# Performance work log

Hardware: AMD Instinct MI355X
Metric: run time of the kernel (lower is better)

Reference implementation:

```python
import jax, jax.numpy as jnp
import numpy as np

N_HF = 128
N_RBF = 50
CUTOFF = 5.0
L = 3          # n_interactions
MAX_Z = 100
N_NODES = 30   # atoms per molecule
B = 1024       # molecules
N = B * N_NODES          # 30720 atoms
E = B * N_NODES * (N_NODES - 1)  # 890880 edges
N_REACT = 256
LOG2 = float(np.log(2.0))


def ssp(x):  # shifted softplus
    return jax.nn.softplus(x) - LOG2


def setup_inputs() -> dict:
    key = jax.random.key(0)
    ks = jax.random.split(key, 24)
    s = 0.02
    z = jax.random.randint(ks[0], (N,), 0, MAX_Z)
    coord = jax.random.normal(ks[1], (N, 3), jnp.float32) * 3.0
    # fully-connected edges within each molecule
    base = np.arange(N_NODES)
    row_l, col_l = np.meshgrid(base, base, indexing='ij')
    mask = row_l != col_l
    row_l, col_l = row_l[mask], col_l[mask]  # [n_nodes*(n_nodes-1)]
    offs = (np.arange(B) * N_NODES)[:, None]
    row = (offs + row_l[None, :]).reshape(-1)
    col = (offs + col_l[None, :]).reshape(-1)
    edge_index = jnp.asarray(np.stack([row, col]), jnp.int32)  # [2,E]
    atom_mask = jnp.ones((N, 1), jnp.float32)
    edge_mask = jnp.ones((E, 1), jnp.float32)
    reaction_indexes = jax.random.randint(ks[2], (B,), 0, N_REACT)
    reaction_indexes_signs = jnp.ones((B,), jnp.float32)
    # parameters
    emb = (jax.random.normal(ks[3], (MAX_Z, N_HF), jnp.float32)).at[0].set(0.0)  # padding_idx=0
    p = lambda k, shp: jax.random.normal(k, shp, jnp.float32) * s
    params = dict(
        in2f_W=p(ks[4], (L, N_HF, N_HF)),
        f_W1=p(ks[5], (L, N_RBF, N_HF)), f_b1=jnp.zeros((L, N_HF), jnp.float32),
        f_W2=p(ks[6], (L, N_HF, N_HF)), f_b2=jnp.zeros((L, N_HF), jnp.float32),
        o_W1=p(ks[7], (L, N_HF, N_HF)), o_b1=jnp.zeros((L, N_HF), jnp.float32),
        o_W2=p(ks[8], (L, N_HF, N_HF)), o_b2=jnp.zeros((L, N_HF), jnp.float32),
        dec_W1=p(ks[9], (N_HF, N_HF // 2)), dec_b1=jnp.zeros((N_HF // 2,), jnp.float32),
        dec_W2=p(ks[10], (N_HF // 2, 1)), dec_b2=jnp.zeros((1,), jnp.float32),
    )
    return dict(z=z, coord=coord, edge_index=edge_index, atom_mask=atom_mask,
                edge_mask=edge_mask, reaction_indexes=reaction_indexes,
                reaction_indexes_signs=reaction_indexes_signs, emb=emb,
                n_nodes=N_NODES, n_reactions=N_REACT, **params)


def reference(z, coord, edge_index, atom_mask, edge_mask, reaction_indexes,
              reaction_indexes_signs, emb, in2f_W, f_W1, f_b1, f_W2, f_b2,
              o_W1, o_b1, o_W2, o_b2, dec_W1, dec_b1, dec_W2, dec_b2,
              n_nodes, n_reactions):
    row, col = edge_index[0], edge_index[1]
    radial = jnp.linalg.norm(coord[row] - coord[col], axis=1)  # [E]
    h = emb[z]  # [N, n_hf]
    # GaussianRBF expansion
    offsets = jnp.linspace(0.0, CUTOFF, N_RBF)
    coeff = -0.5 / (offsets[1] - offsets[0]) ** 2
    rbf = jnp.exp(coeff * (radial[:, None] - offsets[None, :]) ** 2)  # [E, n_rbf]
    rbf = rbf * edge_mask
    # Cosine cutoff
    dc = 0.5 * (jnp.cos(radial * jnp.pi / CUTOFF) + 1.0) * (radial < CUTOFF)
    dist_cut = dc[:, None] * edge_mask  # [E,1]
    n_atoms = h.shape[0]
    for l in range(L):
        xf = h @ in2f_W[l]                                      # in2f (no bias)
        Wij = ssp(rbf @ f_W1[l] + f_b1[l]) @ f_W2[l] + f_b2[l]  # filter network
        Wij = Wij * dist_cut
        x_ij = xf[col] * Wij                                    # gather + multiply
        m = jax.ops.segment_sum(x_ij, row, num_segments=n_atoms)  # scatter-add
        m = ssp(m @ o_W1[l] + o_b1[l]) @ o_W2[l] + o_b2[l]      # f2out
        h = h + m
    h = h * atom_mask
    h = h.reshape(-1, n_nodes, N_HF).sum(axis=1)                # [B, n_hf]
    temp = ssp(h @ dec_W1 + dec_b1) @ dec_W2 + dec_b2           # [B, 1]
    pred = jnp.zeros((n_reactions,), jnp.float32).at[reaction_indexes].add(
        temp[:, 0] * reaction_indexes_signs)
    return pred
```

## Files before the change

kernel.cpp:

```cpp
#include <hip/hip_runtime.h>
#include <math.h>

#define NHF 128
#define NRBF 50
#define LAYERS 3
#define CUTOFF_F 5.0f
#define STEP_F (CUTOFF_F/49.0f)
#define LOG2_F 0.6931471805599453f
#define PI_F 3.14159265358979323846f
#define TBL 4096
#define TROWS (TBL+1)
#define TINV ((float)TBL / CUTOFF_F)

typedef __attribute__((ext_vector_type(8))) _Float16 fp16x8;
typedef __attribute__((ext_vector_type(4))) float f32x4;
typedef _Float16 f16x2 __attribute__((ext_vector_type(2)));

static __device__ __forceinline__ unsigned short f2h(float f){
    return __builtin_bit_cast(unsigned short, (_Float16)f);
}
static __device__ __forceinline__ unsigned packh(float lo, float hi){
    return (unsigned)f2h(lo) | ((unsigned)f2h(hi) << 16);
}
static __device__ __forceinline__ float sspf(float x){
    float t = exp2f(-fabsf(x) * 1.44269504f);
    return fmaxf(x, 0.0f) + 0.69314718f * (log2f(1.0f + t) - 1.0f);
}
static __device__ __forceinline__ float4 ld4(const float* p){ return *reinterpret_cast<const float4*>(p); }

__global__ __launch_bounds__(256) void k_pack(const float* __restrict__ in2f_W, const float* __restrict__ o_W1,
                                              const float* __restrict__ o_W2, uint4* __restrict__ Wp){
    int tid = blockIdx.x * 256 + threadIdx.x;
    if (tid >= 9 * 2048) return;
    int g = tid >> 11;
    int rem = tid & 2047;
    int s = rem >> 9;
    int f = (rem >> 6) & 7;
    int l = rem & 63;
    int layer = g / 3, type = g % 3;
    const float* src = (type == 0 ? in2f_W : (type == 1 ? o_W1 : o_W2)) + (size_t)layer * NHF * NHF;
    int row0 = s * 32 + ((l >> 4) << 3);
    int col  = (f << 4) + (l & 15);
    unsigned p0, p1, p2, p3;
    p0 = (unsigned)f2h(src[(row0+0)*NHF + col]) | ((unsigned)f2h(src[(row0+1)*NHF + col]) << 16);
    p1 = (unsigned)f2h(src[(row0+2)*NHF + col]) | ((unsigned)f2h(src[(row0+3)*NHF + col]) << 16);
    p2 = (unsigned)f2h(src[(row0+4)*NHF + col]) | ((unsigned)f2h(src[(row0+5)*NHF + col]) << 16);
    p3 = (unsigned)f2h(src[(row0+6)*NHF + col]) | ((unsigned)f2h(src[(row0+7)*NHF + col]) << 16);
    Wp[tid] = make_uint4(p0, p1, p2, p3);
}

__global__ __launch_bounds__(256) void k_table(const float* __restrict__ W1, const float* __restrict__ b1,
                                               const float* __restrict__ W2, const float* __restrict__ b2,
                                               unsigned short* __restrict__ Th){
    __shared__ float rbfL[2][4][52];
    __shared__ float hidL[2][4][128];
    int l = blockIdx.y;
    int tid = threadIdx.x;
    int g = tid >> 7, c = tid & 127;
    const float* W1l = W1 + (size_t)l * NRBF * NHF;
    const float* W2l = W2 + (size_t)l * NHF * NHF;
    int t0 = blockIdx.x * 8 + g * 4;
    const float coeff = -0.5f / (STEP_F * STEP_F) * 1.44269504f;
    const float dr = CUTOFF_F / (float)TBL;
    if (c < NRBF){
        float off = c * STEP_F;
        #pragma unroll
        for (int i = 0; i < 4; i++){
            int t = t0 + i; if (t > TBL) t = TBL;
            float d = t * dr - off;
            rbfL[g][i][c] = exp2f(coeff * d * d);
        }
    }
    __syncthreads();
    float acc[4];
    float bc = b1[l * NHF + c];
    #pragma unroll
    for (int i = 0; i < 4; i++) acc[i] = bc;
    #pragma unroll 5
    for (int j = 0; j < NRBF; j++){
        float wv = W1l[j * NHF + c];
        #pragma unroll
        for (int i = 0; i < 4; i++) acc[i] = fmaf(rbfL[g][i][j], wv, acc[i]);
    }
    #pragma unroll
    for (int i = 0; i < 4; i++) hidL[g][i][c] = sspf(acc[i]);
    __syncthreads();
    float b2c = b2[l * NHF + c];
    #pragma unroll
    for (int i = 0; i < 4; i++) acc[i] = b2c;
    #pragma unroll 4
    for (int j = 0; j < NHF; j++){
        float wv = W2l[j * NHF + c];
        #pragma unroll
        for (int i = 0; i < 4; i++) acc[i] = fmaf(hidL[g][i][j], wv, acc[i]);
    }
    #pragma unroll
    for (int i = 0; i < 4; i++){
        int t = t0 + i; if (t > TBL) t = TBL;
        float r = t * dr;
        float dc = (t >= TBL) ? 0.0f : 0.5f * (cosf(r * (PI_F / CUTOFF_F)) + 1.0f);
        float v = acc[i] * dc;
        Th[((size_t)l * TROWS + t) * NHF + c] = f2h(v);
    }
}

static __device__ __forceinline__ fp16x8 ldX(const unsigned* A_u, int rfbase, int ks, int l){
    int row = rfbase + (l & 15);
    int wc = ks * 16 + ((l >> 4) << 2);
    uint4 v = *reinterpret_cast<const uint4*>(&A_u[row * 64 + (wc ^ ((row & 7) << 2))]);
    return __builtin_bit_cast(fp16x8, v);
}
static __device__ __forceinline__ fp16x8 ldW(const uint4* __restrict__ Wp, int g, int ks, int cfg, int l){
    uint4 v = Wp[(((g << 2) + ks) * 8 + cfg) * 64 + l];
    return __builtin_bit_cast(fp16x8, v);
}

template<int EPI>
static __device__ __forceinline__ void gemm_phase(const uint4* __restrict__ Wp, int g,
                                                  const unsigned* A_u, uint2* D2,
                                                  float hreg[2][2][4], const float* __restrict__ bias,
                                                  int w, int l){
    f32x4 acc00 = {0,0,0,0}, acc01 = {0,0,0,0}, acc10 = {0,0,0,0}, acc11 = {0,0,0,0};
    #pragma unroll
    for (int ks = 0; ks < 4; ks++){
        fp16x8 wa0 = ldW(Wp, g, ks, w * 2 + 0, l);
        fp16x8 wa1 = ldW(Wp, g, ks, w * 2 + 1, l);
        fp16x8 xb0 = ldX(A_u, 0, ks, l);
        fp16x8 xb1 = ldX(A_u, 16, ks, l);
        acc00 = __builtin_amdgcn_mfma_f32_16x16x32_f16(wa0, xb0, acc00, 0, 0, 0);
        acc01 = __builtin_amdgcn_mfma_f32_16x16x32_f16(wa0, xb1, acc01, 0, 0, 0);
        acc10 = __builtin_amdgcn_mfma_f32_16x16x32_f16(wa1, xb0, acc10, 0, 0, 0);
        acc11 = __builtin_amdgcn_mfma_f32_16x16x32_f16(wa1, xb1, acc11, 0, 0, 0);
    }
    #pragma unroll
    for (int chf = 0; chf < 2; chf++){
        int ch0 = (w * 2 + chf) * 16 + ((l >> 4) << 2);
        float4 bv = {0,0,0,0};
        if (EPI >= 1) bv = ld4(bias + ch0);
        #pragma unroll
        for (int af = 0; af < 2; af++){
            f32x4 a = (chf == 0) ? (af == 0 ? acc00 : acc01) : (af == 0 ? acc10 : acc11);
            int atom = af * 16 + (l & 15);
            float v0 = a[0] + bv.x, v1 = a[1] + bv.y, v2 = a[2] + bv.z, v3 = a[3] + bv.w;
            if (EPI == 1){ v0 = sspf(v0); v1 = sspf(v1); v2 = sspf(v2); v3 = sspf(v3); }
            if (EPI == 2){
                v0 += hreg[chf][af][0]; hreg[chf][af][0] = v0;
                v1 += hreg[chf][af][1]; hreg[chf][af][1] = v1;
                v2 += hreg[chf][af][2]; hreg[chf][af][2] = v2;
                v3 += hreg[chf][af][3]; hreg[chf][af][3] = v3;
            }
            D2[(atom << 5) + (((ch0 >> 2) ^ ((atom & 7) << 1)))] = make_uint2(packh(v0, v1), packh(v2, v3));
        }
    }
}

__global__ __launch_bounds__(256, 4) void k_mega(const int* __restrict__ z, const float* __restrict__ coord,
                                                 const float* __restrict__ emask, const float* __restrict__ amask,
                                                 const float* __restrict__ emb,
                                                 const uint4* __restrict__ Wp,
                                                 const float* __restrict__ o_b1, const float* __restrict__ o_b2,
                                                 const unsigned* __restrict__ Tb,
                                                 const float* __restrict__ dW1, const float* __restrict__ db1,
                                                 const float* __restrict__ dW2, const float* __restrict__ db2,
                                                 float* __restrict__ tempv, int nn){
    __shared__ __align__(16) unsigned hbf[32 * 64];
    __shared__ __align__(16) unsigned xfb[32 * 64];
    __shared__ __align__(16) unsigned mbu[32 * 64];
    __shared__ __align__(16) int pkE[32 * 32];
    __shared__ int      cntL[32];
    __shared__ int      cntQ[8];
    __shared__ int      zL[32];
    __shared__ unsigned maskL[32];
    __shared__ float    cxyz[96];
    __shared__ float    amL[32];
    __shared__ float    hsb[NHF];

    int mol = blockIdx.x;
    int tid = threadIdx.x;
    int w = tid >> 6, l = tid & 63;
    int molA = mol * nn;
    int km = nn - 1;
    int ne = nn * km;

    uint2* hbf2 = reinterpret_cast<uint2*>(hbf);
    uint2* xfb2 = reinterpret_cast<uint2*>(xfb);

    if (tid < 32){ maskL[tid] = 0u; cntL[tid] = 0; }
    if (tid < 3 * nn) cxyz[tid] = coord[(size_t)molA * 3 + tid];
    if (tid < 32)     amL[tid] = (tid < nn) ? amask[molA + tid] : 0.0f;
    if (tid < 32)     zL[tid]  = (tid < nn) ? z[molA + tid] : 0;
    __syncthreads();
    for (int e = tid; e < ne; e += 256){
        if (emask[(size_t)molA * km + e] != 0.0f){
            int a = e / km, k = e - a * km;
            atomicOr(&maskL[a], 1u << k);
        }
    }

    float hreg[2][2][4];
    #pragma unroll
    for (int chf = 0; chf < 2; chf++){
        int ch0 = (w * 2 + chf) * 16 + ((l >> 4) << 2);
        #pragma unroll
        for (int af = 0; af < 2; af++){
            int atom = af * 16 + (l & 15);
            float4 v = {0,0,0,0};
            if (atom < nn) v = ld4(emb + (size_t)zL[atom] * NHF + ch0);
            hreg[chf][af][0] = v.x; hreg[chf][af][1] = v.y;
            hreg[chf][af][2] = v.z; hreg[chf][af][3] = v.w;
            hbf2[(atom << 5) + (((ch0 >> 2) ^ ((atom & 7) << 1)))] = make_uint2(packh(v.x, v.y), packh(v.z, v.w));
        }
    }
    __syncthreads();

    if (tid < nn){
        int ai = tid;
        unsigned msk = maskL[ai];
        float ax = cxyz[ai*3], ay = cxyz[ai*3+1], az = cxyz[ai*3+2];
        int cnt = 0;
        for (int k = 0; k < km; k++){
            int nb = k + (k >= ai ? 1 : 0);
            float dx = ax - cxyz[nb*3], dy = ay - cxyz[nb*3+1], dz = az - cxyz[nb*3+2];
            float r = sqrtf(dx*dx + dy*dy + dz*dz);
            int t = (int)(r * TINV + 0.5f);
            if (((msk >> k) & 1u) && t < TBL){
                pkE[ai * 32 + cnt] = nb | (t << 8);
                cnt++;
            }
        }
        cntL[ai] = cnt;
    }
    __syncthreads();
    if (tid < 32){
        int b4 = tid & ~3;
        int m0 = cntL[b4], m1 = cntL[b4+1], m2 = cntL[b4+2], m3 = cntL[b4+3];
        int mx = max(max(m0, m1), max(m2, m3));
        mx = (mx + 3) & ~3;
        for (int k = cntL[tid]; k < mx; k++) pkE[tid * 32 + k] = (TBL << 8);
        if (!(tid & 3)) cntQ[tid >> 2] = mx;
    }
    __syncthreads();

    int j16 = l & 15, g16 = l >> 4;
    for (int L = 0; L < LAYERS; L++){
        gemm_phase<0>(Wp, L * 3 + 0, hbf, xfb2, hreg, o_b1, w, l);
        __syncthreads();
        const char* Tlj = (const char*)(Tb + (size_t)L * TROWS * 64) + (j16 << 4);
        for (int q = w; q < 8; q += 4){
            int a = (q << 2) + g16;
            int n4 = cntQ[q] >> 2;
            const int4* pe4 = reinterpret_cast<const int4*>(&pkE[a * 32]);
            float accf[8] = {0,0,0,0,0,0,0,0};
            for (int k4 = 0; k4 < n4; k4++){
                int4 pv = pe4[k4];
                #pragma unroll
                for (int jj = 0; jj < 4; jj++){
                    int p = (jj == 0) ? pv.x : (jj == 1) ? pv.y : (jj == 2) ? pv.z : pv.w;
                    uint4 tw = *reinterpret_cast<const uint4*>(Tlj + (p & ~0xFF));
                    int ca = p & 31;
                    uint4 xw = *reinterpret_cast<const uint4*>(&xfb[(ca << 6) + ((j16 ^ (ca & 7)) << 2)]);
                    f16x2 t0 = __builtin_bit_cast(f16x2, tw.x), t1 = __builtin_bit_cast(f16x2, tw.y);
                    f16x2 t2 = __builtin_bit_cast(f16x2, tw.z), t3 = __builtin_bit_cast(f16x2, tw.w);
                    f16x2 x0 = __builtin_bit_cast(f16x2, xw.x), x1 = __builtin_bit_cast(f16x2, xw.y);
                    f16x2 x2 = __builtin_bit_cast(f16x2, xw.z), x3 = __builtin_bit_cast(f16x2, xw.w);
                    accf[0] += (float)t0[0] * (float)x0[0];
                    accf[1] += (float)t0[1] * (float)x0[1];
                    accf[2] += (float)t1[0] * (float)x1[0];
                    accf[3] += (float)t1[1] * (float)x1[1];
                    accf[4] += (float)t2[0] * (float)x2[0];
                    accf[5] += (float)t2[1] * (float)x2[1];
                    accf[6] += (float)t3[0] * (float)x3[0];
                    accf[7] += (float)t3[1] * (float)x3[1];
                }
            }
            *reinterpret_cast<uint4*>(&mbu[(a << 6) + ((j16 ^ (a & 7)) << 2)]) =
                make_uint4(packh(accf[0], accf[1]), packh(accf[2], accf[3]),
                           packh(accf[4], accf[5]), packh(accf[6], accf[7]));
        }
        __syncthreads();
        gemm_phase<1>(Wp, L * 3 + 1, mbu, xfb2, hreg, o_b1 + L * NHF, w, l);
        __syncthreads();
        gemm_phase<2>(Wp, L * 3 + 2, xfb, hbf2, hreg, o_b2 + L * NHF, w, l);
        __syncthreads();
    }

    {
        float s[2][4];
        #pragma unroll
        for (int chf = 0; chf < 2; chf++)
            #pragma unroll
            for (int r = 0; r < 4; r++)
                s[chf][r] = hreg[chf][0][r] * amL[l & 15] + hreg[chf][1][r] * amL[16 + (l & 15)];
        #pragma unroll
        for (int o = 1; o < 16; o <<= 1){
            #pragma unroll
            for (int chf = 0; chf < 2; chf++)
                #pragma unroll
                for (int r = 0; r < 4; r++)
                    s[chf][r] += __shfl_xor(s[chf][r], o);
        }
        if (!(l & 15)){
            #pragma unroll
            for (int chf = 0; chf < 2; chf++)
                #pragma unroll
                for (int r = 0; r < 4; r++)
                    hsb[(w * 2 + chf) * 16 + ((l >> 4) << 2) + r] = s[chf][r];
        }
    }
    __syncthreads();
    {
        float* red = (float*)pkE;
        int o = tid & 63, part = tid >> 6;
        float u = 0.0f;
        #pragma unroll 8
        for (int c = part * 32; c < part * 32 + 32; c++)
            u = fmaf(hsb[c], dW1[c * 64 + o], u);
        red[part * 64 + o] = u;
    }
    __syncthreads();
    if (tid < 64){
        float u = ((float*)pkE)[tid] + ((float*)pkE)[64 + tid] + ((float*)pkE)[128 + tid]
                + ((float*)pkE)[192 + tid] + db1[tid];
        float p = sspf(u) * dW2[tid];
        #pragma unroll
        for (int o = 32; o > 0; o >>= 1) p += __shfl_down(p, o);
        if (tid == 0) tempv[mol] = p + db2[0];
    }
}

__global__ __launch_bounds__(256) void k_pred(const float* __restrict__ tempv, const int* __restrict__ ridx,
                                              const float* __restrict__ rsign, float* __restrict__ pred,
                                              int nmol, int nreact){
    extern __shared__ float sh[];
    float* tv = sh;
    int*   ri = (int*)(sh + nmol);
    int tid = threadIdx.x;
    for (int i = tid; i < nmol; i += 256){
        tv[i] = tempv[i] * rsign[i];
        ri[i] = ridx[i];
    }
    __syncthreads();
    int r = blockIdx.x * 256 + tid;
    if (r >= nreact) return;
    float s = 0.0f;
    int i = 0;
    for (; i + 8 <= nmol; i += 8){
        #pragma unroll
        for (int j = 0; j < 8; j++){
            float v = tv[i + j];
            s += (ri[i + j] == r) ? v : 0.0f;
        }
    }
    for (; i < nmol; i++)
        s += (ri[i] == r) ? tv[i] : 0.0f;
    pred[r] = s;
}

extern "C" void kernel_launch(void* const* d_in, const int* in_sizes, int n_in,
                              void* d_out, int out_size, void* d_ws, size_t ws_size,
                              hipStream_t stream){
    const int*   z      = (const int*)  d_in[0];
    const float* coord  = (const float*)d_in[1];
    const float* amask  = (const float*)d_in[3];
    const float* emask  = (const float*)d_in[4];
    const int*   ridx   = (const int*)  d_in[5];
    const float* rsign  = (const float*)d_in[6];
    const float* emb    = (const float*)d_in[7];
    const float* in2f_W = (const float*)d_in[10];
    const float* f_W1   = (const float*)d_in[11];
    const float* f_b1   = (const float*)d_in[12];
    const float* f_W2   = (const float*)d_in[13];
    const float* f_b2   = (const float*)d_in[14];
    const float* o_W1   = (const float*)d_in[15];
    const float* o_b1   = (const float*)d_in[16];
    const float* o_W2   = (const float*)d_in[17];
    const float* o_b2   = (const float*)d_in[18];
    const float* dW1    = (const float*)d_in[19];
    const float* db1    = (const float*)d_in[20];
    const float* dW2    = (const float*)d_in[21];
    const float* db2    = (const float*)d_in[22];

    const int N  = in_sizes[0];
    const int B  = in_sizes[5];
    const int nn = N / B;
    (void)n_in; (void)ws_size;

    uint4*    Wp    = (uint4*)d_ws;
    unsigned* Tb    = (unsigned*)((char*)d_ws + 9 * 2048 * 16);
    float*    tempv = (float*)((char*)Tb + (size_t)LAYERS * TROWS * 256);

    k_pack <<<72, 256, 0, stream>>>(in2f_W, o_W1, o_W2, Wp);
    k_table<<<dim3((TROWS + 7) / 8, LAYERS), 256, 0, stream>>>(f_W1, f_b1, f_W2, f_b2,
                                                               (unsigned short*)Tb);
    k_mega <<<B, 256, 0, stream>>>(z, coord, emask, amask, emb, Wp, o_b1, o_b2, Tb,
                                   dW1, db1, dW2, db2, tempv, nn);
    k_pred <<<(out_size + 255) / 256, 256, B * 8, stream>>>(tempv, ridx, rsign,
                                                            (float*)d_out, B, out_size);
}
```

Measured before the change: 102.2 us.

## Fuse weight-pack into table kernel and interleave two atom streams per wave

The weight-packing kernel is folded into the filter-table kernel as an extra grid row, which removes one kernel launch. In the message-passing loop, each wave now handles two atoms (a and a+16) at once with independent accumulators. Previously it looped over two quads one after the other. This exposes more independent table and LDS loads for latency hiding. Padding counts are now taken as the max over 8 atoms instead of 4, so there can be more wasted padded iterations. There is also more register pressure.

```diff
diff --git a/kernel.cpp b/kernel.cpp
--- a/kernel.cpp
+++ b/kernel.cpp
@@ -28,32 +28,48 @@
 }
 static __device__ __forceinline__ float4 ld4(const float* p){ return *reinterpret_cast<const float4*>(p); }
 
-__global__ __launch_bounds__(256) void k_pack(const float* __restrict__ in2f_W, const float* __restrict__ o_W1,
-                                              const float* __restrict__ o_W2, uint4* __restrict__ Wp){
-    int tid = blockIdx.x * 256 + threadIdx.x;
-    if (tid >= 9 * 2048) return;
-    int g = tid >> 11;
-    int rem = tid & 2047;
-    int s = rem >> 9;
-    int f = (rem >> 6) & 7;
-    int l = rem & 63;
-    int layer = g / 3, type = g % 3;
-    const float* src = (type == 0 ? in2f_W : (type == 1 ? o_W1 : o_W2)) + (size_t)layer * NHF * NHF;
-    int row0 = s * 32 + ((l >> 4) << 3);
-    int col  = (f << 4) + (l & 15);
-    unsigned p0, p1, p2, p3;
-    p0 = (unsigned)f2h(src[(row0+0)*NHF + col]) | ((unsigned)f2h(src[(row0+1)*NHF + col]) << 16);
-    p1 = (unsigned)f2h(src[(row0+2)*NHF + col]) | ((unsigned)f2h(src[(row0+3)*NHF + col]) << 16);
-    p2 = (unsigned)f2h(src[(row0+4)*NHF + col]) | ((unsigned)f2h(src[(row0+5)*NHF + col]) << 16);
-    p3 = (unsigned)f2h(src[(row0+6)*NHF + col]) | ((unsigned)f2h(src[(row0+7)*NHF + col]) << 16);
-    Wp[tid] = make_uint4(p0, p1, p2, p3);
+static __device__ __forceinline__ void acc8(float acc[8], uint4 tw, uint4 xw){
+    f16x2 t0 = __builtin_bit_cast(f16x2, tw.x), t1 = __builtin_bit_cast(f16x2, tw.y);
+    f16x2 t2 = __builtin_bit_cast(f16x2, tw.z), t3 = __builtin_bit_cast(f16x2, tw.w);
+    f16x2 x0 = __builtin_bit_cast(f16x2, xw.x), x1 = __builtin_bit_cast(f16x2, xw.y);
+    f16x2 x2 = __builtin_bit_cast(f16x2, xw.z), x3 = __builtin_bit_cast(f16x2, xw.w);
+    acc[0] += (float)t0[0] * (float)x0[0];
+    acc[1] += (float)t0[1] * (float)x0[1];
+    acc[2] += (float)t1[0] * (float)x1[0];
+    acc[3] += (float)t1[1] * (float)x1[1];
+    acc[4] += (float)t2[0] * (float)x2[0];
+    acc[5] += (float)t2[1] * (float)x2[1];
+    acc[6] += (float)t3[0] * (float)x3[0];
+    acc[7] += (float)t3[1] * (float)x3[1];
 }
 
 __global__ __launch_bounds__(256) void k_table(const float* __restrict__ W1, const float* __restrict__ b1,
                                                const float* __restrict__ W2, const float* __restrict__ b2,
-                                               unsigned short* __restrict__ Th){
+                                               unsigned short* __restrict__ Th,
+                                               const float* __restrict__ in2f_W, const float* __restrict__ o_W1,
+                                               const float* __restrict__ o_W2, uint4* __restrict__ Wp){
     __shared__ float rbfL[2][4][52];
     __shared__ float hidL[2][4][128];
+    if (blockIdx.y == LAYERS){
+        int tid = blockIdx.x * 256 + threadIdx.x;
+        if (tid >= 9 * 2048) return;
+        int g = tid >> 11;
+        int rem = tid & 2047;
+        int s = rem >> 9;
+        int f = (rem >> 6) & 7;
+        int l = rem & 63;
+        int layer = g / 3, type = g % 3;
+        const float* src = (type == 0 ? in2f_W : (type == 1 ? o_W1 : o_W2)) + (size_t)layer * NHF * NHF;
+        int row0 = s * 32 + ((l >> 4) << 3);
+        int col  = (f << 4) + (l & 15);
+        unsigned p0, p1, p2, p3;
+        p0 = (unsigned)f2h(src[(row0+0)*NHF + col]) | ((unsigned)f2h(src[(row0+1)*NHF + col]) << 16);
+        p1 = (unsigned)f2h(src[(row0+2)*NHF + col]) | ((unsigned)f2h(src[(row0+3)*NHF + col]) << 16);
+        p2 = (unsigned)f2h(src[(row0+4)*NHF + col]) | ((unsigned)f2h(src[(row0+5)*NHF + col]) << 16);
+        p3 = (unsigned)f2h(src[(row0+6)*NHF + col]) | ((unsigned)f2h(src[(row0+7)*NHF + col]) << 16);
+        Wp[tid] = make_uint4(p0, p1, p2, p3);
+        return;
+    }
     int l = blockIdx.y;
     int tid = threadIdx.x;
     int g = tid >> 7, c = tid & 127;
@@ -168,7 +184,7 @@
     __shared__ __align__(16) unsigned mbu[32 * 64];
     __shared__ __align__(16) int pkE[32 * 32];
     __shared__ int      cntL[32];
-    __shared__ int      cntQ[8];
+    __shared__ int      cntQ[4];
     __shared__ int      zL[32];
     __shared__ unsigned maskL[32];
     __shared__ float    cxyz[96];
@@ -232,12 +248,14 @@
     }
     __syncthreads();
     if (tid < 32){
-        int b4 = tid & ~3;
-        int m0 = cntL[b4], m1 = cntL[b4+1], m2 = cntL[b4+2], m3 = cntL[b4+3];
-        int mx = max(max(m0, m1), max(m2, m3));
+        int qp = (tid >> 2) & 3;
+        int mx = 0;
+        #pragma unroll
+        for (int i = 0; i < 4; i++)
+            mx = max(mx, max(cntL[qp * 4 + i], cntL[qp * 4 + 16 + i]));
         mx = (mx + 3) & ~3;
         for (int k = cntL[tid]; k < mx; k++) pkE[tid * 32 + k] = (TBL << 8);
-        if (!(tid & 3)) cntQ[tid >> 2] = mx;
+        if (tid == qp * 4) cntQ[qp] = mx;
     }
     __syncthreads();
 
@@ -246,36 +264,36 @@
         gemm_phase<0>(Wp, L * 3 + 0, hbf, xfb2, hreg, o_b1, w, l);
         __syncthreads();
         const char* Tlj = (const char*)(Tb + (size_t)L * TROWS * 64) + (j16 << 4);
-        for (int q = w; q < 8; q += 4){
-            int a = (q << 2) + g16;
-            int n4 = cntQ[q] >> 2;
-            const int4* pe4 = reinterpret_cast<const int4*>(&pkE[a * 32]);
-            float accf[8] = {0,0,0,0,0,0,0,0};
+        {
+            int aA = (w << 2) + g16;
+            int aB = aA + 16;
+            int n4 = cntQ[w] >> 2;
+            const int4* peA4 = reinterpret_cast<const int4*>(&pkE[aA * 32]);
+            const int4* peB4 = reinterpret_cast<const int4*>(&pkE[aB * 32]);
+            float accA[8] = {0,0,0,0,0,0,0,0};
+            float accB[8] = {0,0,0,0,0,0,0,0};
             for (int k4 = 0; k4 < n4; k4++){
-                int4 pv = pe4[k4];
+                int4 pa = peA4[k4];
+                int4 pb = peB4[k4];
                 #pragma unroll
                 for (int jj = 0; jj < 4; jj++){
-                    int p = (jj == 0) ? pv.x : (jj == 1) ? pv.y : (jj == 2) ? pv.z : pv.w;
-                    uint4 tw = *reinterpret_cast<const uint4*>(Tlj + (p & ~0xFF));
-                    int ca = p & 31;
-                    uint4 xw = *reinterpret_cast<const uint4*>(&xfb[(ca << 6) + ((j16 ^ (ca & 7)) << 2)]);
-                    f16x2 t0 = __builtin_bit_cast(f16x2, tw.x), t1 = __builtin_bit_cast(f16x2, tw.y);
-                    f16x2 t2 = __builtin_bit_cast(f16x2, tw.z), t3 = __builtin_bit_cast(f16x2, tw.w);
-                    f16x2 x0 = __builtin_bit_cast(f16x2, xw.x), x1 = __builtin_bit_cast(f16x2, xw.y);
-                    f16x2 x2 = __builtin_bit_cast(f16x2, xw.z), x3 = __builtin_bit_cast(f16x2, xw.w);
-                    accf[0] += (float)t0[0] * (float)x0[0];
-                    accf[1] += (float)t0[1] * (float)x0[1];
-                    accf[2] += (float)t1[0] * (float)x1[0];
-                    accf[3] += (float)t1[1] * (float)x1[1];
-                    accf[4] += (float)t2[0] * (float)x2[0];
-                    accf[5] += (float)t2[1] * (float)x2[1];
-                    accf[6] += (float)t3[0] * (float)x3[0];
-                    accf[7] += (float)t3[1] * (float)x3[1];
+                    int pA_ = (jj == 0) ? pa.x : (jj == 1) ? pa.y : (jj == 2) ? pa.z : pa.w;
+                    int pB_ = (jj == 0) ? pb.x : (jj == 1) ? pb.y : (jj == 2) ? pb.z : pb.w;
+                    uint4 twA = *reinterpret_cast<const uint4*>(Tlj + (pA_ & ~0xFF));
+                    uint4 twB = *reinterpret_cast<const uint4*>(Tlj + (pB_ & ~0xFF));
+                    int caA = pA_ & 31, caB = pB_ & 31;
+                    uint4 xwA = *reinterpret_cast<const uint4*>(&xfb[(caA << 6) + ((j16 ^ (caA & 7)) << 2)]);
+                    uint4 xwB = *reinterpret_cast<const uint4*>(&xfb[(caB << 6) + ((j16 ^ (caB & 7)) << 2)]);
+                    acc8(accA, twA, xwA);
+                    acc8(accB, twB, xwB);
                 }
             }
-            *reinterpret_cast<uint4*>(&mbu[(a << 6) + ((j16 ^ (a & 7)) << 2)]) =
-                make_uint4(packh(accf[0], accf[1]), packh(accf[2], accf[3]),
-                           packh(accf[4], accf[5]), packh(accf[6], accf[7]));
+            *reinterpret_cast<uint4*>(&mbu[(aA << 6) + ((j16 ^ (aA & 7)) << 2)]) =
+                make_uint4(packh(accA[0], accA[1]), packh(accA[2], accA[3]),
+                           packh(accA[4], accA[5]), packh(accA[6], accA[7]));
+            *reinterpret_cast<uint4*>(&mbu[(aB << 6) + ((j16 ^ (aB & 7)) << 2)]) =
+                make_uint4(packh(accB[0], accB[1]), packh(accB[2], accB[3]),
+                           packh(accB[4], accB[5]), packh(accB[6], accB[7]));
         }
         __syncthreads();
         gemm_phase<1>(Wp, L * 3 + 1, mbu, xfb2, hreg, o_b1 + L * NHF, w, l);
@@ -389,9 +407,9 @@
     unsigned* Tb    = (unsigned*)((char*)d_ws + 9 * 2048 * 16);
     float*    tempv = (float*)((char*)Tb + (size_t)LAYERS * TROWS * 256);
 
-    k_pack <<<72, 256, 0, stream>>>(in2f_W, o_W1, o_W2, Wp);
-    k_table<<<dim3((TROWS + 7) / 8, LAYERS), 256, 0, stream>>>(f_W1, f_b1, f_W2, f_b2,
-                                                               (unsigned short*)Tb);
+    k_table<<<dim3((TROWS + 7) / 8, LAYERS + 1), 256, 0, stream>>>(f_W1, f_b1, f_W2, f_b2,
+                                                                   (unsigned short*)Tb,
+                                                                   in2f_W, o_W1, o_W2, Wp);
     k_mega <<<B, 256, 0, stream>>>(z, coord, emask, amask, emb, Wp, o_b1, o_b2, Tb,
                                    dW1, db1, dW2, db2, tempv, nn);
     k_pred <<<(out_size + 255) / 256, 256, B * 8, stream>>>(tempv, ridx, rsign,
```

After: 107.1 us. 1.05x slower.
